# Kernel tuning notes

Hardware: AMD Instinct MI355X
Metric: run time of the kernel (lower is better)

## Reference

```python
import jax, jax.numpy as jnp
import numpy as np

THRESH = 1.0
SLOPE = 25.0  # fast_sigmoid surrogate slope
B, T, C_IN = 64, 512, 32
HID, TS, K = 128, 4, 3
C_OUT = HID * TS

@jax.custom_vjp
def spike_fn(x):
    # Heaviside forward, fast-sigmoid surrogate backward (matches snntorch surrogate.fast_sigmoid(slope=25))
    return (x > 0).astype(x.dtype)

def _spike_fwd(x):
    return spike_fn(x), x

def _spike_bwd(x, g):
    return (g / (SLOPE * jnp.abs(x) + 1.0) ** 2,)

spike_fn.defvjp(_spike_fwd, _spike_bwd)


def setup_inputs() -> dict:
    key = jax.random.key(0)
    ks = jax.random.split(key, 4)
    return {
        "x": jax.random.normal(ks[0], (B, T, C_IN), jnp.float32),
        "conv_w": jax.random.normal(ks[1], (C_OUT, C_IN, K), jnp.float32) / np.sqrt(C_IN * K).astype(np.float32),
        "conv_b": jax.random.normal(ks[2], (C_OUT,), jnp.float32) * 0.01,
        "bn_gamma": jnp.ones((C_OUT,), jnp.float32),
        "bn_beta": jnp.zeros((C_OUT,), jnp.float32),
        "bn_mean": jax.random.normal(ks[3], (C_OUT,), jnp.float32) * 0.1,
        "bn_var": jnp.ones((C_OUT,), jnp.float32),
        "lif_beta": jnp.full((HID,), 0.9, jnp.float32),
    }


def reference(x, conv_w, conv_b, bn_gamma, bn_beta, bn_mean, bn_var, lif_beta):
    # Conv1d(input -> hidden*Ts, k=3, pad=1): x (B,T,C) -> NCH layout
    h = jax.lax.conv_general_dilated(
        x.transpose(0, 2, 1), conv_w, (1,), [(K // 2, K // 2)],
        dimension_numbers=("NCH", "OIH", "NCH"))  # (B, C_OUT, T)
    h = h + conv_b[None, :, None]
    # BatchNorm1d in eval mode (running stats)
    scale = bn_gamma * jax.lax.rsqrt(bn_var + 1e-5)
    h = (h - bn_mean[None, :, None]) * scale[None, :, None] + bn_beta[None, :, None]
    # (B, C_OUT, T) -> (B, T, Ts, HID) -> (Ts*T, B, HID) time-major spike input
    h = h.transpose(0, 2, 1).reshape(B, T * TS, HID).transpose(1, 0, 2)

    beta = jnp.clip(lif_beta, 0.0, 1.0)

    def step(mem, h_t):
        # snntorch Leaky (reset_mechanism='subtract'): reset from previous mem, detached
        reset = jax.lax.stop_gradient((mem > THRESH).astype(mem.dtype))
        mem = beta * mem + h_t - reset * THRESH
        spk = spike_fn(mem - THRESH)
        return mem, (spk, mem)

    mem0 = jnp.zeros((B, HID), x.dtype)
    _, (spk_rec, mem_rec) = jax.lax.scan(step, mem0, h)
    return spk_rec, mem_rec  # each (Ts*T, B, HID)
```

## Files before the change

kernel.cpp:

```cpp
#include <hip/hip_runtime.h>

#define T_LEN 512
#define CIN   32
#define HIDN  128
#define TSUB  4
#define NB    64
#define TT    64
#define NT2   2048
#define COLS  8192

__global__ __launch_bounds__(256) void conv_bn_kernel(
    const float* __restrict__ x,
    const float* __restrict__ w,
    const float* __restrict__ cb,
    const float* __restrict__ gam,
    const float* __restrict__ bet,
    const float* __restrict__ mean,
    const float* __restrict__ var,
    float* __restrict__ h)
{
    __shared__ float xs[66 * 36];
    __shared__ float ws[128 * 100];
    __shared__ float scs[128];
    __shared__ float bbs[128];

    const int t0  = blockIdx.x * TT;
    const int s   = blockIdx.y;
    const int b   = blockIdx.z;
    const int tid = threadIdx.x;

    for (int idx = tid; idx < 66 * 32; idx += 256) {
        int r = idx >> 5, ci = idx & 31;
        int t = t0 + r - 1;
        xs[r * 36 + ci] = (t >= 0 && t < T_LEN) ? x[(b * T_LEN + t) * CIN + ci] : 0.0f;
    }
    for (int idx = tid; idx < 128 * 96; idx += 256) {
        int row = idx / 96, j = idx - row * 96;
        int k = j >> 5, i = j & 31;
        ws[row * 100 + j] = w[(s * HIDN + row) * (CIN * 3) + i * 3 + k];
    }
    if (tid < 128) {
        int c = s * HIDN + tid;
        float sc = gam[c] * rsqrtf(var[c] + 1e-5f);
        scs[tid] = sc;
        bbs[tid] = (cb[c] - mean[c]) * sc + bet[c];
    }
    __syncthreads();

    const int tc = tid & 31;
    const int tt = tid >> 5;

    float acc[4][8];
#pragma unroll
    for (int a = 0; a < 4; ++a)
#pragma unroll
        for (int q = 0; q < 8; ++q) acc[a][q] = 0.0f;

    for (int j0 = 0; j0 < 96; j0 += 4) {
        const int k  = j0 >> 5;
        const int i0 = j0 & 31;
        float4 wv[4];
#pragma unroll
        for (int cc = 0; cc < 4; ++cc)
            wv[cc] = *reinterpret_cast<const float4*>(&ws[(tc + cc * 32) * 100 + j0]);
#pragma unroll
        for (int tq = 0; tq < 8; ++tq) {
            float4 xv = *reinterpret_cast<const float4*>(&xs[(tt * 8 + tq + k) * 36 + i0]);
#pragma unroll
            for (int cc = 0; cc < 4; ++cc) {
                acc[cc][tq] = fmaf(wv[cc].x, xv.x, acc[cc][tq]);
                acc[cc][tq] = fmaf(wv[cc].y, xv.y, acc[cc][tq]);
                acc[cc][tq] = fmaf(wv[cc].z, xv.z, acc[cc][tq]);
                acc[cc][tq] = fmaf(wv[cc].w, xv.w, acc[cc][tq]);
            }
        }
    }

#pragma unroll
    for (int cc = 0; cc < 4; ++cc) {
        const int hid = tc + cc * 32;
        const float sc = scs[hid], bb = bbs[hid];
#pragma unroll
        for (int tq = 0; tq < 8; ++tq) {
            const int t = t0 + tt * 8 + tq;
            h[((t * TSUB + s) * NB + b) * HIDN + hid] = fmaf(acc[cc][tq], sc, bb);
        }
    }
}

__global__ __launch_bounds__(64) void lif_scan_kernel(
    const float* __restrict__ h,
    const float* __restrict__ lifb,
    float* __restrict__ out)
{
    const int col = blockIdx.x * 64 + threadIdx.x;
    const int hid = col & (HIDN - 1);
    float beta = lifb[hid];
    beta = fminf(fmaxf(beta, 0.0f), 1.0f);

    float* __restrict__ spk  = out;
    float* __restrict__ memo = out + (size_t)NT2 * COLS;

    float mem = 0.0f;
    constexpr int PF = 32;
    float hv[PF];
#pragma unroll
    for (int i = 0; i < PF; ++i) hv[i] = h[i * COLS + col];

    for (int t0 = 0; t0 < NT2; t0 += PF) {
        float hn[PF];
        if (t0 + PF < NT2) {
#pragma unroll
            for (int i = 0; i < PF; ++i) hn[i] = h[(t0 + PF + i) * COLS + col];
        }
#pragma unroll
        for (int i = 0; i < PF; ++i) {
            const float reset = (mem > 1.0f) ? 1.0f : 0.0f;
            mem = __fsub_rn(__fadd_rn(__fmul_rn(beta, mem), hv[i]), reset);
            const int idx = (t0 + i) * COLS + col;
            spk[idx]  = (mem > 1.0f) ? 1.0f : 0.0f;
            memo[idx] = mem;
        }
#pragma unroll
        for (int i = 0; i < PF; ++i) hv[i] = hn[i];
    }
}

extern "C" void kernel_launch(void* const* d_in, const int* in_sizes, int n_in,
                              void* d_out, int out_size, void* d_ws, size_t ws_size,
                              hipStream_t stream) {
    const float* x    = (const float*)d_in[0];
    const float* w    = (const float*)d_in[1];
    const float* cb   = (const float*)d_in[2];
    const float* gam  = (const float*)d_in[3];
    const float* bet  = (const float*)d_in[4];
    const float* mean = (const float*)d_in[5];
    const float* var  = (const float*)d_in[6];
    const float* lifb = (const float*)d_in[7];

    float* h = (float*)d_ws;

    dim3 gA(T_LEN / TT, TSUB, NB);
    conv_bn_kernel<<<gA, 256, 0, stream>>>(x, w, cb, gam, bet, mean, var, h);

    lif_scan_kernel<<<COLS / 64, 64, 0, stream>>>(h, lifb, (float*)d_out);
}
```

Measured before the change: 290.7 us.

## Split LIF scan into checkpoint pass and parallel chunked replay pass

The single sequential scan over 128 blocks of 64 threads is split in two. Pass 1 runs the recurrence and stores only a membrane checkpoint every 32 steps. Pass 2 launches one block per chunk and column group, so thousands of blocks recompute the chunks in parallel from the checkpoints and write the full spike and membrane outputs. The aim is to fix the low occupancy and write-bandwidth limit of the original scan, at the cost of reading h twice and adding a third kernel launch.

```diff
diff --git a/kernel.cpp b/kernel.cpp
--- a/kernel.cpp
+++ b/kernel.cpp
@@ -8,6 +8,8 @@
 #define TT    64
 #define NT2   2048
 #define COLS  8192
+#define CHUNK 32
+#define NCHUNK (NT2 / CHUNK)
 
 __global__ __launch_bounds__(256) void conv_bn_kernel(
     const float* __restrict__ x,
@@ -88,7 +90,7 @@
     }
 }
 
-__global__ __launch_bounds__(64) void lif_scan_kernel(
+__global__ __launch_bounds__(64) void lif_pass1_kernel(
     const float* __restrict__ h,
     const float* __restrict__ lifb,
     float* __restrict__ out)
@@ -98,11 +100,10 @@
     float beta = lifb[hid];
     beta = fminf(fmaxf(beta, 0.0f), 1.0f);
 
-    float* __restrict__ spk  = out;
     float* __restrict__ memo = out + (size_t)NT2 * COLS;
 
     float mem = 0.0f;
-    constexpr int PF = 32;
+    constexpr int PF = 64;
     float hv[PF];
 #pragma unroll
     for (int i = 0; i < PF; ++i) hv[i] = h[i * COLS + col];
@@ -117,7 +118,49 @@
         for (int i = 0; i < PF; ++i) {
             const float reset = (mem > 1.0f) ? 1.0f : 0.0f;
             mem = __fsub_rn(__fadd_rn(__fmul_rn(beta, mem), hv[i]), reset);
-            const int idx = (t0 + i) * COLS + col;
+            if ((i & (CHUNK - 1)) == CHUNK - 1) {
+                const int t = t0 + i;
+                if (t < NT2 - 1) memo[t * COLS + col] = mem;
+            }
+        }
+#pragma unroll
+        for (int i = 0; i < PF; ++i) hv[i] = hn[i];
+    }
+}
+
+__global__ __launch_bounds__(256) void lif_pass2_kernel(
+    const float* __restrict__ h,
+    const float* __restrict__ lifb,
+    float* __restrict__ out)
+{
+    const int chunk = blockIdx.y;
+    const int col   = blockIdx.x * 256 + threadIdx.x;
+    const int hid   = col & (HIDN - 1);
+    float beta = lifb[hid];
+    beta = fminf(fmaxf(beta, 0.0f), 1.0f);
+
+    float* __restrict__ spk  = out;
+    float* __restrict__ memo = out + (size_t)NT2 * COLS;
+
+    const int tbase = chunk * CHUNK;
+    float mem = (chunk == 0) ? 0.0f : memo[(tbase - 1) * COLS + col];
+
+    constexpr int PF = 16;
+    float hv[PF];
+#pragma unroll
+    for (int i = 0; i < PF; ++i) hv[i] = h[(tbase + i) * COLS + col];
+
+    for (int tt = 0; tt < CHUNK; tt += PF) {
+        float hn[PF];
+        if (tt + PF < CHUNK) {
+#pragma unroll
+            for (int i = 0; i < PF; ++i) hn[i] = h[(tbase + tt + PF + i) * COLS + col];
+        }
+#pragma unroll
+        for (int i = 0; i < PF; ++i) {
+            const float reset = (mem > 1.0f) ? 1.0f : 0.0f;
+            mem = __fsub_rn(__fadd_rn(__fmul_rn(beta, mem), hv[i]), reset);
+            const int idx = (tbase + tt + i) * COLS + col;
             spk[idx]  = (mem > 1.0f) ? 1.0f : 0.0f;
             memo[idx] = mem;
         }
@@ -143,5 +186,8 @@
     dim3 gA(T_LEN / TT, TSUB, NB);
     conv_bn_kernel<<<gA, 256, 0, stream>>>(x, w, cb, gam, bet, mean, var, h);
 
-    lif_scan_kernel<<<COLS / 64, 64, 0, stream>>>(h, lifb, (float*)d_out);
+    lif_pass1_kernel<<<COLS / 64, 64, 0, stream>>>(h, lifb, (float*)d_out);
+
+    dim3 gC(COLS / 256, NCHUNK);
+    lif_pass2_kernel<<<gC, 256, 0, stream>>>(h, lifb, (float*)d_out);
 }
```

After: 288.1 us. No clear change (-0.9%).
